# Performance work log

Measured on AMD Instinct MI355X. Metric: run time of the kernel, lower is better.

The kernel has to match this reference:

```python
import jax, jax.numpy as jnp
import numpy as np

NUM_CLASSES = 7
B = 14336
D = 512
H_KDE = 0.2          # sklearn KernelDensity(bandwidth=0.2, kernel='gaussian')
KERNEL_MUL = 2.0
KERNEL_NUM = 5
BN_EPS = 1e-5


def _pairwise_sqdist(a, b):
    # ||a_i - b_j||^2 via gram trick; avoids the [n,n,d] broadcast tensor the torch code builds
    an = jnp.sum(a * a, axis=-1)
    bn = jnp.sum(b * b, axis=-1)
    d2 = an[:, None] + bn[None, :] - 2.0 * (a @ b.T)
    return jnp.maximum(d2, 0.0)


def _multi_kernel(total):
    # sum of KERNEL_NUM Gaussian kernels, bandwidths 1.25 * 2^i (bandwidth=5 / 2^(5//2))
    d2 = _pairwise_sqdist(total, total)
    bw0 = 5.0 / (KERNEL_MUL ** (KERNEL_NUM // 2))
    k = jnp.zeros_like(d2)
    for i in range(KERNEL_NUM):  # small fixed loop, avoids [5,n,n] intermediate
        k = k + jnp.exp(-d2 / (bw0 * (KERNEL_MUL ** i)))
    return k


def _mmd(src, tgt):
    m = src.shape[0]
    k = _multi_kernel(jnp.concatenate([src, tgt], axis=0))
    return jnp.mean(k[:m, :m] + k[m:, m:] - k[:m, m:] - k[m:, :m])


def _kde_weight(class_feats):
    # sklearn gaussian KDE: log p(x_i) = logsumexp_j(-||x_i-x_j||^2 / (2 h^2)) - log m - (d/2) log(2 pi h^2)
    # volume v = sum_i 1 / log p(x_i); weight = 1 / (v + 1e-5)
    C, m, d = class_feats.shape
    log_norm = -0.5 * d * jnp.log(2.0 * jnp.pi * (H_KDE ** 2)) - jnp.log(jnp.float32(m))

    def one(f):
        d2 = _pairwise_sqdist(f, f)
        logp = jax.nn.logsumexp(-d2 / (2.0 * (H_KDE ** 2)), axis=1) + log_norm
        return jnp.sum(1.0 / logp)

    v = jax.vmap(one)(class_feats)
    return 1.0 / (v + 1e-5)


def setup_inputs() -> dict:
    key = jax.random.key(0)
    k1, k2 = jax.random.split(key)
    fea = jax.random.normal(k1, (B, D), dtype=jnp.float32) * 0.05
    W_fc = jax.random.normal(k2, (NUM_CLASSES, D), dtype=jnp.float32) * 0.02
    gamma = jnp.ones((NUM_CLASSES,), dtype=jnp.float32)
    beta = jnp.zeros((NUM_CLASSES,), dtype=jnp.float32)
    # balanced, contiguous class blocks so per-class splits are static reshapes
    targets = jnp.repeat(jnp.arange(NUM_CLASSES, dtype=jnp.int32), B // NUM_CLASSES)
    return {"fea": fea, "W_fc": W_fc, "gamma": gamma, "beta": beta, "targets": targets}


def reference(fea, W_fc, gamma, beta, targets):
    Bn, d = fea.shape
    C = NUM_CLASSES
    m = Bn // C

    # out = BatchNorm1d(fc(fea)) in train mode (biased batch stats)
    logits = fea @ W_fc.T                              # [B, C]
    mu = jnp.mean(logits, axis=0)
    var = jnp.var(logits, axis=0)
    out = gamma * (logits - mu) / jnp.sqrt(var + BN_EPS) + beta

    # split_feature_makeLD with balanced contiguous targets -> static reshape
    cf = fea.reshape(C, m, d)                          # [C, m, D]

    # KDE density weights: computed on detached numpy features in the original -> stop_gradient
    w = jax.lax.stop_gradient(_kde_weight(cf))         # [C]

    def per_class(i):
        src = cf[i]
        # remove_element concatenates classes 0..i-1, i+1..C-1 in order;
        # first m rows of that = class 0 (class 1 when i == 0)
        tgt = cf[jnp.where(i > 0, 0, 1)]
        return _mmd(src, tgt)

    losses = jax.vmap(per_class)(jnp.arange(C))        # [C]
    affinity_loss = -jnp.sum(losses * w)
    return (out, affinity_loss)
```

## Files before the change

### kernel.cpp

```cpp
#include <hip/hip_runtime.h>

#define B_ROWS 14336
#define D_DIM  512
#define C_CLS  7
#define M_CLS  2048

typedef __attribute__((ext_vector_type(4))) float f32x4;

#define FP8_SCALE 64.0f
#define INV_2S2   (2.0f / 4096.0f)

typedef const __attribute__((address_space(1))) char gchar_t;
typedef __attribute__((address_space(3))) char lchar_t;

__device__ __forceinline__ void gload16(const char* g, char* l) {
  __builtin_amdgcn_global_load_lds((gchar_t*)g, (lchar_t*)l, 16, 0, 0);
}

__global__ __launch_bounds__(256) void k_prep(const float* __restrict__ fea,
                                              const float* __restrict__ W,
                                              char* __restrict__ f8p,
                                              float* __restrict__ an,
                                              float* __restrict__ logits,
                                              float* __restrict__ zb) {
  int t = threadIdx.x, wave = t >> 6, lane = t & 63;
  if (blockIdx.x == 0 && t < 64) zb[t] = 0.f;
  __shared__ char lrow[16 * 528];

  int r0 = blockIdx.x * 16;
#pragma unroll
  for (int k = 0; k < 4; ++k) {
    int rl = wave * 4 + k;
    int row = r0 + rl;
    const float4* fr4 = (const float4*)(fea + (size_t)row * D_DIM);
    float4 v0 = fr4[lane * 2], v1 = fr4[lane * 2 + 1];

    float p[8];
#pragma unroll
    for (int c = 0; c < 7; ++c) {
      const float4* w4 = (const float4*)(W + c * D_DIM);
      float4 q0 = w4[lane * 2], q1 = w4[lane * 2 + 1];
      p[c] = v0.x * q0.x + v0.y * q0.y + v0.z * q0.z + v0.w * q0.w +
             v1.x * q1.x + v1.y * q1.y + v1.z * q1.z + v1.w * q1.w;
    }
    p[7] = v0.x * v0.x + v0.y * v0.y + v0.z * v0.z + v0.w * v0.w +
           v1.x * v1.x + v1.y * v1.y + v1.z * v1.z + v1.w * v1.w;

#pragma unroll
    for (int c = 0; c < 8; ++c) {
      p[c] += __shfl_xor(p[c], 1);
      p[c] += __shfl_xor(p[c], 2);
      p[c] += __shfl_xor(p[c], 4);
    }
    int v = lane & 7;
    float y = p[0];
    y = (v == 1) ? p[1] : y;
    y = (v == 2) ? p[2] : y;
    y = (v == 3) ? p[3] : y;
    y = (v == 4) ? p[4] : y;
    y = (v == 5) ? p[5] : y;
    y = (v == 6) ? p[6] : y;
    y = (v == 7) ? p[7] : y;
    y += __shfl_xor(y, 8);
    y += __shfl_xor(y, 16);
    y += __shfl_xor(y, 32);
    if (lane < 7) logits[row * 7 + lane] = y;
    else if (lane == 7) an[row] = y;

    int w0 = __builtin_amdgcn_cvt_pk_fp8_f32(v0.x * FP8_SCALE, v0.y * FP8_SCALE, 0, 0);
    w0     = __builtin_amdgcn_cvt_pk_fp8_f32(v0.z * FP8_SCALE, v0.w * FP8_SCALE, w0, 1);
    int w1 = __builtin_amdgcn_cvt_pk_fp8_f32(v1.x * FP8_SCALE, v1.y * FP8_SCALE, 0, 0);
    w1     = __builtin_amdgcn_cvt_pk_fp8_f32(v1.z * FP8_SCALE, v1.w * FP8_SCALE, w1, 1);
    *(int2*)&lrow[rl * 528 + lane * 8] = make_int2(w0, w1);
  }
  __syncthreads();
  int4* outp = (int4*)f8p + (size_t)blockIdx.x * 512;
#pragma unroll
  for (int pi = 0; pi < 2; ++pi) {
    int idx = pi * 256 + t;
    int kp = idx >> 6, l = idx & 63;
    int sr = l & 15, qk = l >> 4;
    int2 lo = *(const int2*)&lrow[sr * 528 + kp * 64 + qk * 8];
    int2 hi = *(const int2*)&lrow[sr * 528 + kp * 64 + 32 + qk * 8];
    outp[idx] = make_int4(lo.x, lo.y, hi.x, hi.y);
  }
}

__global__ __launch_bounds__(512, 2) void k_gram(const char* __restrict__ f8p,
                                                 const float* __restrict__ an,
                                                 const float* __restrict__ logits,
                                                 float* __restrict__ S,
                                                 float* __restrict__ rs_part,
                                                 float* __restrict__ S1,
                                                 float* __restrict__ S2,
                                                 float* __restrict__ aff) {
  int x = blockIdx.x & 7, u = blockIdx.x >> 3;
  int t = threadIdx.x, lane = t & 63, wave = t >> 6;
  if (blockIdx.x == 0 && t == 0) aff[0] = 0.f;

  if (u == 80) {
    if (x >= 7) return;
    int c = x, seg = wave;
    int r0 = seg * 1792;
    float s1 = 0.f, s2 = 0.f;
    for (int j = lane; j < 1792; j += 64) {
      float v = logits[(size_t)(r0 + j) * 7 + c];
      s1 += v;
      s2 += v * v;
    }
#pragma unroll
    for (int o = 1; o < 64; o <<= 1) {
      s1 += __shfl_xor(s1, o);
      s2 += __shfl_xor(s2, o);
    }
    if (lane == 0) { atomicAdd(&S1[c], s1); atomicAdd(&S2[c], s2); }
    return;
  }

  int cls1, cls2, ti, tj, Sidx;
  bool self;
  if (x < 7 && u < 36) {
    int a = 0, r = u;
    while (r > a) { r -= a + 1; ++a; }
    ti = a; tj = r;
    cls1 = x; cls2 = x; Sidx = x; self = true;
  } else {
    int j;
    if (x < 7) j = x * 44 + (u - 36);
    else { if (u >= 76) return; j = 308 + u; }
    int p = j >> 6, t64 = j & 63;
    ti = t64 >> 3; tj = t64 & 7;
    cls1 = p + 1; cls2 = 0; Sidx = 7 + p; self = false;
  }

  __shared__ char ldsA[2][16384];
  __shared__ char ldsB[2][16384];
  __shared__ float bacc[8];

  int R0 = cls1 * 2048 + ti * 256;
  int C0 = cls2 * 2048 + tj * 256;

  const char* gA0 = f8p + ((size_t)(R0 >> 4) + wave * 2)     * 8192 + lane * 16;
  const char* gA1 = f8p + ((size_t)(R0 >> 4) + wave * 2 + 1) * 8192 + lane * 16;
  const char* gB0 = f8p + ((size_t)(C0 >> 4) + wave * 2)     * 8192 + lane * 16;
  const char* gB1 = f8p + ((size_t)(C0 >> 4) + wave * 2 + 1) * 8192 + lane * 16;

  int wr = wave >> 2, wc = wave & 3;
  int q = lane >> 4, s = lane & 15;

  f32x4 acc[8][4];
#pragma unroll
  for (int i = 0; i < 8; ++i)
#pragma unroll
    for (int j = 0; j < 4; ++j)
      acc[i][j] = (f32x4){0.f, 0.f, 0.f, 0.f};

  gload16(gA0, &ldsA[0][(wave * 2) * 1024 + lane * 16]);
  gload16(gA1, &ldsA[0][(wave * 2 + 1) * 1024 + lane * 16]);
  gload16(gB0, &ldsB[0][(wave * 2) * 1024 + lane * 16]);
  gload16(gB1, &ldsB[0][(wave * 2 + 1) * 1024 + lane * 16]);
  __syncthreads();

#define MM16(A0_, A1_, I0_, I1_)                                              \
  do {                                                                        \
    asm volatile("s_waitcnt lgkmcnt(0)" ::: "memory");                        \
    __builtin_amdgcn_sched_barrier(0);                                        \
    __builtin_amdgcn_s_setprio(1);                                            \
    _Pragma("unroll")                                                         \
    for (int j_ = 0; j_ < 4; ++j_)                                            \
      acc[I0_][j_] = __builtin_amdgcn_mfma_f32_16x16x32_fp8_fp8(              \
          A0_.x, bb[j_].x, acc[I0_][j_], 0, 0, 0);                            \
    _Pragma("unroll")                                                         \
    for (int j_ = 0; j_ < 4; ++j_)                                            \
      acc[I1_][j_] = __builtin_amdgcn_mfma_f32_16x16x32_fp8_fp8(              \
          A1_.x, bb[j_].x, acc[I1_][j_], 0, 0, 0);                            \
    _Pragma("unroll")                                                         \
    for (int j_ = 0; j_ < 4; ++j_)                                            \
      acc[I0_][j_] = __builtin_amdgcn_mfma_f32_16x16x32_fp8_fp8(              \
          A0_.y, bb[j_].y, acc[I0_][j_], 0, 0, 0);                            \
    _Pragma("unroll")                                                         \
    for (int j_ = 0; j_ < 4; ++j_)                                            \
      acc[I1_][j_] = __builtin_amdgcn_mfma_f32_16x16x32_fp8_fp8(              \
          A1_.y, bb[j_].y, acc[I1_][j_], 0, 0, 0);                            \
    __builtin_amdgcn_s_setprio(0);                                            \
  } while (0)

#pragma unroll 1
  for (int kt = 0; kt < 8; ++kt) {
    int cur = kt & 1;
    const char* LA = &ldsA[cur][(wr * 8) * 1024 + lane * 16];
    const char* LB = &ldsB[cur][(wc * 4) * 1024 + lane * 16];
    longlong2 a0, a1, bb[4];
    a0 = *(const longlong2*)(LA);
    a1 = *(const longlong2*)(LA + 1024);
#pragma unroll
    for (int j = 0; j < 4; ++j) bb[j] = *(const longlong2*)(LB + j * 1024);
    if (kt < 7) {
      int nb = cur ^ 1;
      gload16(gA0 + (kt + 1) * 1024, &ldsA[nb][(wave * 2) * 1024 + lane * 16]);
      gload16(gA1 + (kt + 1) * 1024, &ldsA[nb][(wave * 2 + 1) * 1024 + lane * 16]);
    }
    MM16(a0, a1, 0, 1);
    a0 = *(const longlong2*)(LA + 2 * 1024);
    a1 = *(const longlong2*)(LA + 3 * 1024);
    if (kt < 7) {
      int nb = cur ^ 1;
      gload16(gB0 + (kt + 1) * 1024, &ldsB[nb][(wave * 2) * 1024 + lane * 16]);
      gload16(gB1 + (kt + 1) * 1024, &ldsB[nb][(wave * 2 + 1) * 1024 + lane * 16]);
    }
    __builtin_amdgcn_s_barrier();
    asm volatile("" ::: "memory");
    MM16(a0, a1, 2, 3);
    a0 = *(const longlong2*)(LA + 4 * 1024);
    a1 = *(const longlong2*)(LA + 5 * 1024);
    __builtin_amdgcn_s_barrier();
    asm volatile("" ::: "memory");
    MM16(a0, a1, 4, 5);
    a0 = *(const longlong2*)(LA + 6 * 1024);
    a1 = *(const longlong2*)(LA + 7 * 1024);
    __builtin_amdgcn_s_barrier();
    asm volatile("" ::: "memory");
    MM16(a0, a1, 6, 7);
    if (kt < 7)
      asm volatile("s_waitcnt vmcnt(0)" ::: "memory");
    __builtin_amdgcn_s_barrier();
    asm volatile("" ::: "memory");
  }
#undef MM16

  bool dg = self && (ti == tj);
  bool mirror = self && (ti > tj);
  float blockAcc = 0.f;
  float colAcc[4] = {0.f, 0.f, 0.f, 0.f};
  float anB_[4];
#pragma unroll
  for (int j = 0; j < 4; ++j) anB_[j] = an[C0 + wc * 64 + j * 16 + s];

#pragma unroll
  for (int i = 0; i < 8; ++i) {
    f32x4 anA_ = *(const f32x4*)&an[R0 + wr * 128 + i * 16 + q * 4];
#pragma unroll
    for (int rg = 0; rg < 4; ++rg) {
      int rl = wr * 128 + i * 16 + q * 4 + rg;
      float aA = anA_[rg];
      float rowAcc = 0.f;
#pragma unroll
      for (int j = 0; j < 4; ++j) {
        int cl = wc * 64 + j * 16 + s;
        float g = acc[i][j][rg];
        float d2 = fmaxf(aA + anB_[j] - g * INV_2S2, 0.f);
        if (dg && rl == cl) d2 = 0.f;
        float e1 = __expf(-0.05f * d2);
        float e2 = e1 * e1, e4 = e2 * e2, e8 = e4 * e4, e16 = e8 * e8;
        blockAcc += e1 + e2 + e4 + e8 + e16;
        if (self) {
          float ek = __expf(-12.5f * d2);
          rowAcc += ek;
          if (mirror) colAcc[j] += ek;
        }
      }
      if (self) {
        rowAcc += __shfl_xor(rowAcc, 1);
        rowAcc += __shfl_xor(rowAcc, 2);
        rowAcc += __shfl_xor(rowAcc, 4);
        rowAcc += __shfl_xor(rowAcc, 8);
        if (s == 0)
          rs_part[(size_t)(R0 + rl) * 48 + tj * 4 + wc] = rowAcc;
      }
    }
  }
  if (mirror) {
#pragma unroll
    for (int j = 0; j < 4; ++j) {
      float v = colAcc[j];
      v += __shfl_xor(v, 16);
      v += __shfl_xor(v, 32);
      if (q == 0)
        rs_part[(size_t)(C0 + wc * 64 + j * 16 + s) * 48 + 32 + ti * 2 + wr] = v;
    }
    blockAcc *= 2.f;
  }
#pragma unroll
  for (int o = 1; o < 64; o <<= 1) blockAcc += __shfl_xor(blockAcc, o);
  if (lane == 0) bacc[wave] = blockAcc;
  __syncthreads();
  if (t == 0) {
    float sB = 0.f;
#pragma unroll
    for (int w = 0; w < 8; ++w) sB += bacc[w];
    atomicAdd(&S[Sidx], sB);
  }
}

__global__ __launch_bounds__(1024) void k_final(const float* __restrict__ logits,
                                                const float* __restrict__ S1,
                                                const float* __restrict__ S2,
                                                const float* __restrict__ gamma,
                                                const float* __restrict__ beta,
                                                const float* __restrict__ rs_part,
                                                const float* __restrict__ S,
                                                float* __restrict__ out) {
  int b = blockIdx.x, t = threadIdx.x;
  if (b < 98) {
    int idx = b * 1024 + t;
    int row = idx / 7;
    int c = idx - row * 7;
    float mu = S1[c] * (1.f / 14336.f);
    float var = S2[c] * (1.f / 14336.f) - mu * mu;
    out[idx] = gamma[c] * (logits[idx] - mu) * rsqrtf(var + 1e-5f) + beta[c];
    return;
  }
  int c = b - 98;
  const float LOG_NORM = 345.9110632f;
  float v = 0.f;
  for (int i = t; i < M_CLS; i += 1024) {
    int bi = i >> 8;
    const float* rp = rs_part + (size_t)(c * M_CLS + i) * 48;
    float rsum = 0.f;
    int nd = 4 * bi + 4;
    for (int k = 0; k < nd; ++k) rsum += rp[k];
    for (int k = 34 + 2 * bi; k < 48; ++k) rsum += rp[k];
    v += 1.f / (logf(rsum) + LOG_NORM);
  }
#pragma unroll
  for (int o = 1; o < 64; o <<= 1) v += __shfl_xor(v, o);
  __shared__ float r[16];
  if ((t & 63) == 0) r[t >> 6] = v;
  __syncthreads();
  if (t == 0) {
    float vs = 0.f;
#pragma unroll
    for (int w = 0; w < 16; ++w) vs += r[w];
    float w = 1.f / (vs + 1e-5f);
    const float inv_m2 = 1.0f / ((float)M_CLS * (float)M_CLS);
    float Ssrc = S[c];
    float Stgt = (c > 0) ? S[0] : S[1];
    float X    = (c > 0) ? S[6 + c] : S[7];
    float mmd = (Ssrc + Stgt - 2.f * X) * inv_m2;
    atomicAdd(&out[100352], -mmd * w);
  }
}

extern "C" void kernel_launch(void* const* d_in, const int* in_sizes, int n_in,
                              void* d_out, int out_size, void* d_ws, size_t ws_size,
                              hipStream_t stream) {
  const float* fea   = (const float*)d_in[0];
  const float* W_fc  = (const float*)d_in[1];
  const float* gamma = (const float*)d_in[2];
  const float* beta  = (const float*)d_in[3];
  float* out = (float*)d_out;

  char* ws = (char*)d_ws;
  char* f8p = ws;
  float* fbase   = (float*)(ws + 7340032);
  float* an      = fbase;
  float* logits  = fbase + 14336;
  float* zb      = fbase + 114688;
  float* S1      = zb;
  float* S2      = zb + 7;
  float* S       = zb + 16;
  float* rs_part = fbase + 114752;

  k_prep <<<896, 256, 0, stream>>>(fea, W_fc, f8p, an, logits, zb);
  k_gram <<<648, 512, 0, stream>>>(f8p, an, logits, S, rs_part, S1, S2,
                                   out + 100352);
  k_final<<<105, 1024, 0, stream>>>(logits, S1, S2, gamma, beta, rs_part, S, out);
}
```

Before: 186.3 us.

## Shrink gram tiles to 128x128 with 256-thread blocks for more parallelism

Cuts the k_gram output tile from 256x256 (8 waves) to 128x128 (4 waves). The grid grows from 648 to 2504 blocks, with launch bounds of 4 blocks per CU, and the triangular self-tile and cross-tile block maps plus the BN-statistics blocks are rebuilt to match. The rs_part row stride grows to 64 and k_final now reads partial row sums as float2 pairs. The goal is better load balance and occupancy across CUs, at the cost of less operand reuse per tile, more global/LDS traffic and more atomics.

```diff
diff --git a/kernel.cpp b/kernel.cpp
--- a/kernel.cpp
+++ b/kernel.cpp
@@ -86,7 +86,7 @@
   }
 }
 
-__global__ __launch_bounds__(512, 2) void k_gram(const char* __restrict__ f8p,
+__global__ __launch_bounds__(256, 4) void k_gram(const char* __restrict__ f8p,
                                                  const float* __restrict__ an,
                                                  const float* __restrict__ logits,
                                                  float* __restrict__ S,
@@ -98,9 +98,12 @@
   int t = threadIdx.x, lane = t & 63, wave = t >> 6;
   if (blockIdx.x == 0 && t == 0) aff[0] = 0.f;
 
-  if (u == 80) {
-    if (x >= 7) return;
-    int c = x, seg = wave;
+  if (u >= 311) {
+    int blk;
+    if (u == 311) blk = x;
+    else { if (x >= 6) return; blk = 8 + x; }
+    int idx = blk * 4 + wave;
+    int c = idx >> 3, seg = idx & 7;
     int r0 = seg * 1792;
     float s1 = 0.f, s2 = 0.f;
     for (int j = lane; j < 1792; j += 64) {
@@ -119,38 +122,38 @@
 
   int cls1, cls2, ti, tj, Sidx;
   bool self;
-  if (x < 7 && u < 36) {
+  if (x < 7 && u < 136) {
     int a = 0, r = u;
     while (r > a) { r -= a + 1; ++a; }
     ti = a; tj = r;
     cls1 = x; cls2 = x; Sidx = x; self = true;
   } else {
     int j;
-    if (x < 7) j = x * 44 + (u - 36);
-    else { if (u >= 76) return; j = 308 + u; }
-    int p = j >> 6, t64 = j & 63;
-    ti = t64 >> 3; tj = t64 & 7;
+    if (x < 7) j = x * 175 + (u - 136);
+    else j = 1225 + u;
+    int p = j >> 8, t256 = j & 255;
+    ti = t256 >> 4; tj = t256 & 15;
     cls1 = p + 1; cls2 = 0; Sidx = 7 + p; self = false;
   }
 
-  __shared__ char ldsA[2][16384];
-  __shared__ char ldsB[2][16384];
-  __shared__ float bacc[8];
-
-  int R0 = cls1 * 2048 + ti * 256;
-  int C0 = cls2 * 2048 + tj * 256;
+  __shared__ char ldsA[2][8192];
+  __shared__ char ldsB[2][8192];
+  __shared__ float bacc[4];
+
+  int R0 = cls1 * 2048 + ti * 128;
+  int C0 = cls2 * 2048 + tj * 128;
 
   const char* gA0 = f8p + ((size_t)(R0 >> 4) + wave * 2)     * 8192 + lane * 16;
   const char* gA1 = f8p + ((size_t)(R0 >> 4) + wave * 2 + 1) * 8192 + lane * 16;
   const char* gB0 = f8p + ((size_t)(C0 >> 4) + wave * 2)     * 8192 + lane * 16;
   const char* gB1 = f8p + ((size_t)(C0 >> 4) + wave * 2 + 1) * 8192 + lane * 16;
 
-  int wr = wave >> 2, wc = wave & 3;
+  int wr = wave >> 1, wc = wave & 1;
   int q = lane >> 4, s = lane & 15;
 
-  f32x4 acc[8][4];
-#pragma unroll
-  for (int i = 0; i < 8; ++i)
+  f32x4 acc[4][4];
+#pragma unroll
+  for (int i = 0; i < 4; ++i)
 #pragma unroll
     for (int j = 0; j < 4; ++j)
       acc[i][j] = (f32x4){0.f, 0.f, 0.f, 0.f};
@@ -188,7 +191,7 @@
 #pragma unroll 1
   for (int kt = 0; kt < 8; ++kt) {
     int cur = kt & 1;
-    const char* LA = &ldsA[cur][(wr * 8) * 1024 + lane * 16];
+    const char* LA = &ldsA[cur][(wr * 4) * 1024 + lane * 16];
     const char* LB = &ldsB[cur][(wc * 4) * 1024 + lane * 16];
     longlong2 a0, a1, bb[4];
     a0 = *(const longlong2*)(LA);
@@ -211,16 +214,6 @@
     __builtin_amdgcn_s_barrier();
     asm volatile("" ::: "memory");
     MM16(a0, a1, 2, 3);
-    a0 = *(const longlong2*)(LA + 4 * 1024);
-    a1 = *(const longlong2*)(LA + 5 * 1024);
-    __builtin_amdgcn_s_barrier();
-    asm volatile("" ::: "memory");
-    MM16(a0, a1, 4, 5);
-    a0 = *(const longlong2*)(LA + 6 * 1024);
-    a1 = *(const longlong2*)(LA + 7 * 1024);
-    __builtin_amdgcn_s_barrier();
-    asm volatile("" ::: "memory");
-    MM16(a0, a1, 6, 7);
     if (kt < 7)
       asm volatile("s_waitcnt vmcnt(0)" ::: "memory");
     __builtin_amdgcn_s_barrier();
@@ -237,11 +230,11 @@
   for (int j = 0; j < 4; ++j) anB_[j] = an[C0 + wc * 64 + j * 16 + s];
 
 #pragma unroll
-  for (int i = 0; i < 8; ++i) {
-    f32x4 anA_ = *(const f32x4*)&an[R0 + wr * 128 + i * 16 + q * 4];
+  for (int i = 0; i < 4; ++i) {
+    f32x4 anA_ = *(const f32x4*)&an[R0 + wr * 64 + i * 16 + q * 4];
 #pragma unroll
     for (int rg = 0; rg < 4; ++rg) {
-      int rl = wr * 128 + i * 16 + q * 4 + rg;
+      int rl = wr * 64 + i * 16 + q * 4 + rg;
       float aA = anA_[rg];
       float rowAcc = 0.f;
 #pragma unroll
@@ -265,7 +258,7 @@
         rowAcc += __shfl_xor(rowAcc, 4);
         rowAcc += __shfl_xor(rowAcc, 8);
         if (s == 0)
-          rs_part[(size_t)(R0 + rl) * 48 + tj * 4 + wc] = rowAcc;
+          rs_part[(size_t)(R0 + rl) * 64 + tj * 2 + wc] = rowAcc;
       }
     }
   }
@@ -276,7 +269,7 @@
       v += __shfl_xor(v, 16);
       v += __shfl_xor(v, 32);
       if (q == 0)
-        rs_part[(size_t)(C0 + wc * 64 + j * 16 + s) * 48 + 32 + ti * 2 + wr] = v;
+        rs_part[(size_t)(C0 + wc * 64 + j * 16 + s) * 64 + 32 + ti * 2 + wr] = v;
     }
     blockAcc *= 2.f;
   }
@@ -284,12 +277,8 @@
   for (int o = 1; o < 64; o <<= 1) blockAcc += __shfl_xor(blockAcc, o);
   if (lane == 0) bacc[wave] = blockAcc;
   __syncthreads();
-  if (t == 0) {
-    float sB = 0.f;
-#pragma unroll
-    for (int w = 0; w < 8; ++w) sB += bacc[w];
-    atomicAdd(&S[Sidx], sB);
-  }
+  if (t == 0)
+    atomicAdd(&S[Sidx], bacc[0] + bacc[1] + bacc[2] + bacc[3]);
 }
 
 __global__ __launch_bounds__(1024) void k_final(const float* __restrict__ logits,
@@ -314,12 +303,19 @@
   const float LOG_NORM = 345.9110632f;
   float v = 0.f;
   for (int i = t; i < M_CLS; i += 1024) {
-    int bi = i >> 8;
-    const float* rp = rs_part + (size_t)(c * M_CLS + i) * 48;
+    int bi = i >> 7;
+    const float* rp = rs_part + (size_t)(c * M_CLS + i) * 64;
     float rsum = 0.f;
-    int nd = 4 * bi + 4;
-    for (int k = 0; k < nd; ++k) rsum += rp[k];
-    for (int k = 34 + 2 * bi; k < 48; ++k) rsum += rp[k];
+    const float2* rpd = (const float2*)rp;
+    for (int k = 0; k <= bi; ++k) {
+      float2 xx = rpd[k];
+      rsum += xx.x + xx.y;
+    }
+    const float2* rpm = (const float2*)(rp + 34 + 2 * bi);
+    for (int k = 0; k < 15 - bi; ++k) {
+      float2 xx = rpm[k];
+      rsum += xx.x + xx.y;
+    }
     v += 1.f / (logf(rsum) + LOG_NORM);
   }
 #pragma unroll
@@ -361,8 +357,8 @@
   float* S       = zb + 16;
   float* rs_part = fbase + 114752;
 
-  k_prep <<<896, 256, 0, stream>>>(fea, W_fc, f8p, an, logits, zb);
-  k_gram <<<648, 512, 0, stream>>>(f8p, an, logits, S, rs_part, S1, S2,
-                                   out + 100352);
+  k_prep <<<896,  256, 0, stream>>>(fea, W_fc, f8p, an, logits, zb);
+  k_gram <<<2504, 256, 0, stream>>>(f8p, an, logits, S, rs_part, S1, S2,
+                                    out + 100352);
   k_final<<<105, 1024, 0, stream>>>(logits, S1, S2, gamma, beta, rs_part, S, out);
 }
```

New measurement: 157.7 us (median of 2 runs). 15.3% less time.
